# Performance work log

Hardware: AMD Instinct MI355X
Metric: run time of the kernel (lower is better)

Reference implementation:

```python
import jax, jax.numpy as jnp
import numpy as np

E = 8            # moe_num_experts
FFN = 8192       # ffn_hidden_size
D = 2048         # d_model
B, T = 1, 4096


def setup_inputs() -> dict:
    key = jax.random.key(0)
    k1, k2, k3, k4 = jax.random.split(key, 4)
    x = jax.random.normal(k1, (B, T, D), dtype=jnp.float32)
    # params stored flat as (E*FFN, D), as in the flax module
    w1 = jax.random.normal(k2, (E * FFN, D), dtype=jnp.float32) * 0.02
    v1 = jax.random.normal(k3, (E * FFN, D), dtype=jnp.float32) * 0.02
    w2 = jax.random.normal(k4, (E * FFN, D), dtype=jnp.float32) * 0.02
    return {"x": x, "w1": w1, "v1": v1, "w2": w2, "expert_idx": 3}


def reference(x, w1, v1, w2, expert_idx):
    # select this expert's weight slabs: (FFN, D) each
    expert_shape = (E, FFN, D)
    ew1 = w1.reshape(expert_shape)[expert_idx]
    ev1 = v1.reshape(expert_shape)[expert_idx]
    ew2 = w2.reshape(expert_shape)[expert_idx]
    # gate and up projections: [B,T,D] x [D,FFN] -> [B,T,FFN]
    x1 = jnp.einsum('btd,fd->btf', x, ew1)
    x2 = jnp.einsum('btd,fd->btf', x, ev1)
    h = jax.nn.silu(x1) * x2
    # down projection (note: matmul with ew2, i.e. contraction over FFN)
    out = jnp.einsum('btf,fd->btd', h, ew2)
    return out
```

## Files before the change

### kernel.cpp

```cpp
#include <hip/hip_runtime.h>

#define E_NUM 8
#define FFN_DIM 8192
#define D_DIM 2048
#define T_DIM 4096

using bf16x8 = __attribute__((ext_vector_type(8))) short;
using f32x4  = __attribute__((ext_vector_type(4))) float;
using u16x8  = __attribute__((ext_vector_type(8))) unsigned short;

__device__ __forceinline__ unsigned short f2bf(float f) {
  union { float f; unsigned int u; } v; v.f = f;
  unsigned int u = v.u;
  unsigned int r = (u + 0x7FFFu + ((u >> 16) & 1u)) >> 16;
  return (unsigned short)r;
}

__device__ __forceinline__ void gload16(const unsigned short* g, const unsigned short* l) {
  __builtin_amdgcn_global_load_lds(
      (const __attribute__((address_space(1))) void*)g,
      (__attribute__((address_space(3))) void*)l, 16, 0, 0);
}

__global__ void convert_kernel(const float* __restrict__ src_base,
                               const int* __restrict__ eidx, long slab,
                               unsigned short* __restrict__ dst, long n) {
  const float* src = src_base + (long)(*eidx) * slab;
  long stride = (long)gridDim.x * blockDim.x;
  for (long i = (long)blockIdx.x * blockDim.x + threadIdx.x; i * 8 < n; i += stride) {
    long e = i * 8;
    const float4* p = (const float4*)(src + e);
    float4 f0 = p[0], f1 = p[1];
    u16x8 o;
    o[0] = f2bf(f0.x); o[1] = f2bf(f0.y); o[2] = f2bf(f0.z); o[3] = f2bf(f0.w);
    o[4] = f2bf(f1.x); o[5] = f2bf(f1.y); o[6] = f2bf(f1.z); o[7] = f2bf(f1.w);
    *(u16x8*)(dst + e) = o;
  }
}

__global__ __launch_bounds__(512) void transpose_kernel(
    const float* __restrict__ w2, const int* __restrict__ eidx,
    unsigned short* __restrict__ dst) {
  __shared__ unsigned short tile[64][72];
  const float* src = w2 + (long)(*eidx) * (long)FFN_DIM * D_DIM;
  const int tid = threadIdx.x;
  int d0 = blockIdx.x << 6;
  int f0 = blockIdx.y << 6;
#pragma unroll
  for (int p = 0; p < 2; ++p) {
    int f = p * 32 + (tid >> 4);
    int dc = (tid & 15) * 4;
    float4 v = *(const float4*)(src + (long)(f0 + f) * D_DIM + d0 + dc);
    tile[f][dc + 0] = f2bf(v.x); tile[f][dc + 1] = f2bf(v.y);
    tile[f][dc + 2] = f2bf(v.z); tile[f][dc + 3] = f2bf(v.w);
  }
  __syncthreads();
  int d = tid >> 3;
  int fc = (tid & 7) * 8;
  u16x8 o;
#pragma unroll
  for (int j = 0; j < 8; ++j) o[j] = tile[fc + j][d];
  *(u16x8*)(dst + (long)(d0 + d) * FFN_DIM + f0 + fc) = o;
}

#define VMCNT8 asm volatile("s_waitcnt vmcnt(8)" ::: "memory")
#define VMCNT6 asm volatile("s_waitcnt vmcnt(6)" ::: "memory")
#define VMCNT5 asm volatile("s_waitcnt vmcnt(5)" ::: "memory")
#define VMCNT3 asm volatile("s_waitcnt vmcnt(3)" ::: "memory")
#define VMCNT0 asm volatile("s_waitcnt vmcnt(0)" ::: "memory")
#define BAR asm volatile("s_waitcnt lgkmcnt(0)\n\ts_barrier" ::: "memory")
#define PRIO1 __builtin_amdgcn_s_setprio(1)
#define PRIO0 __builtin_amdgcn_s_setprio(0)

__global__ __launch_bounds__(512, 2) void gemm1_silu(
    const unsigned short* __restrict__ Xb,
    const unsigned short* __restrict__ W1b,
    const unsigned short* __restrict__ V1b,
    unsigned short* __restrict__ Hb) {
  __shared__ __align__(16) unsigned short sA[2 * 16384];
  __shared__ __align__(16) unsigned short sB1[2 * 8192];
  __shared__ __align__(16) unsigned short sB2[2 * 8192];

  const int tid = threadIdx.x;
  const int wv = tid >> 6, l = tid & 63;
  const int wm = wv >> 2, wn = wv & 3;
  const int kq = l >> 4, lr = l & 15;
  const int bsw = (blockIdx.x & 7) * 128 + (blockIdx.x >> 3);
  const int m0 = (bsw >> 6) << 8;
  const int n0 = (bsw & 63) << 7;

  const int rsub = tid >> 3;
  const int sslot8 = ((tid & 7) ^ ((tid >> 3) & 7)) << 3;
  const unsigned short* gA  = Xb  + (long)(m0 + rsub) * D_DIM + sslot8;
  const unsigned short* gB1 = W1b + (long)(n0 + rsub) * D_DIM + sslot8;
  const unsigned short* gB2 = V1b + (long)(n0 + rsub) * D_DIM + sslot8;

#define STG1(gbase, r_, tc_, lbase) \
  gload16((gbase) + (long)((r_) * 64) * D_DIM + (tc_), (lbase) + (r_) * 4096 + wv * 512)

  int aoffA[4], aoffB[4], boff[2];
#pragma unroll
  for (int j = 0; j < 4; ++j) {
    int rowA = wm * 64 + j * 16 + lr;
    aoffA[j] = rowA * 64 + ((kq ^ (rowA & 7)) << 3);
    int rowB = 128 + wm * 64 + j * 16 + lr;
    aoffB[j] = rowB * 64 + ((kq ^ (rowB & 7)) << 3);
  }
#pragma unroll
  for (int g = 0; g < 2; ++g) {
    int row = wn * 32 + g * 16 + lr;
    boff[g] = row * 64 + ((kq ^ (row & 7)) << 3);
  }

  f32x4 acc1[8][2], acc2[8][2];
  f32x4 z = {0.f, 0.f, 0.f, 0.f};
#pragma unroll
  for (int f = 0; f < 8; ++f)
#pragma unroll
    for (int g = 0; g < 2; ++g) { acc1[f][g] = z; acc2[f][g] = z; }

  bf16x8 aA[4][2], aB[4][2], b1[2][2], b2[2][2];

  STG1(gB1, 0, 0, sB1); STG1(gB1, 1, 0, sB1);
  STG1(gA, 0, 0, sA); STG1(gA, 1, 0, sA); STG1(gA, 2, 0, sA); STG1(gA, 3, 0, sA);
  STG1(gB2, 0, 0, sB2); STG1(gB2, 1, 0, sB2);
  STG1(gB1, 0, 64, sB1 + 8192); STG1(gB1, 1, 64, sB1 + 8192);
  STG1(gA, 0, 64, sA + 16384); STG1(gA, 1, 64, sA + 16384);
  STG1(gA, 2, 64, sA + 16384); STG1(gA, 3, 64, sA + 16384);
  STG1(gB2, 0, 64, sB2 + 8192); STG1(gB2, 1, 64, sB2 + 8192);
  VMCNT8;
  BAR;
#pragma unroll
  for (int j = 0; j < 4; ++j) {
    aA[j][0] = *(const bf16x8*)(sA + aoffA[j]);
    aA[j][1] = *(const bf16x8*)(sA + (aoffA[j] ^ 32));
  }
#pragma unroll
  for (int g = 0; g < 2; ++g) {
    b1[g][0] = *(const bf16x8*)(sB1 + boff[g]);
    b1[g][1] = *(const bf16x8*)(sB1 + (boff[g] ^ 32));
  }
  BAR;

  const int NT = D_DIM / 64;
  for (int t = 0; t < NT; ++t) {
    const int db = t & 1, nx = db ^ 1;
    const unsigned short* Acur  = sA  + db * 16384;
    const unsigned short* Anxt  = sA  + nx * 16384;
    const unsigned short* B1nxt = sB1 + nx * 8192;
    const unsigned short* B2cur = sB2 + db * 8192;
    unsigned short* AcurW  = (unsigned short*)sA  + db * 16384;
    unsigned short* B1curW = (unsigned short*)sB1 + db * 8192;
    unsigned short* B2curW = (unsigned short*)sB2 + db * 8192;
    const int p1ok = (t + 1 < NT), p2ok = (t + 2 < NT);
    const int tc2 = (t + 2) << 6;

#pragma unroll
    for (int j = 0; j < 4; ++j) {
      aB[j][0] = *(const bf16x8*)(Acur + aoffB[j]);
      aB[j][1] = *(const bf16x8*)(Acur + (aoffB[j] ^ 32));
    }
    if (p2ok) { STG1(gB1, 0, tc2, B1curW); STG1(gB1, 1, tc2, B1curW); }
    PRIO1;
#pragma unroll
    for (int j = 0; j < 4; ++j)
#pragma unroll
      for (int g = 0; g < 2; ++g) {
        acc1[j][g] = __builtin_amdgcn_mfma_f32_16x16x32_bf16(aA[j][0], b1[g][0], acc1[j][g], 0, 0, 0);
        acc1[j][g] = __builtin_amdgcn_mfma_f32_16x16x32_bf16(aA[j][1], b1[g][1], acc1[j][g], 0, 0, 0);
      }
    PRIO0;
    BAR;

#pragma unroll
    for (int g = 0; g < 2; ++g) {
      b2[g][0] = *(const bf16x8*)(B2cur + boff[g]);
      b2[g][1] = *(const bf16x8*)(B2cur + (boff[g] ^ 32));
    }
    if (p2ok) { STG1(gA, 0, tc2, AcurW); STG1(gA, 1, tc2, AcurW); STG1(gA, 2, tc2, AcurW); }
    PRIO1;
#pragma unroll
    for (int j = 0; j < 4; ++j)
#pragma unroll
      for (int g = 0; g < 2; ++g) {
        acc1[4 + j][g] = __builtin_amdgcn_mfma_f32_16x16x32_bf16(aB[j][0], b1[g][0], acc1[4 + j][g], 0, 0, 0);
        acc1[4 + j][g] = __builtin_amdgcn_mfma_f32_16x16x32_bf16(aB[j][1], b1[g][1], acc1[4 + j][g], 0, 0, 0);
      }
    PRIO0;
    if (p2ok) { VMCNT5; } else if (p1ok) { VMCNT0; }
    BAR;

    if (p2ok) { STG1(gA, 3, tc2, AcurW); STG1(gB2, 0, tc2, B2curW); STG1(gB2, 1, tc2, B2curW); }
    PRIO1;
#pragma unroll
    for (int j = 0; j < 4; ++j)
#pragma unroll
      for (int g = 0; g < 2; ++g) {
        acc2[j][g] = __builtin_amdgcn_mfma_f32_16x16x32_bf16(aA[j][0], b2[g][0], acc2[j][g], 0, 0, 0);
        acc2[j][g] = __builtin_amdgcn_mfma_f32_16x16x32_bf16(aA[j][1], b2[g][1], acc2[j][g], 0, 0, 0);
      }
    PRIO0;
    if (p1ok) {
#pragma unroll
      for (int j = 0; j < 4; ++j) {
        aA[j][0] = *(const bf16x8*)(Anxt + aoffA[j]);
        aA[j][1] = *(const bf16x8*)(Anxt + (aoffA[j] ^ 32));
      }
    }
    BAR;

    PRIO1;
#pragma unroll
    for (int j = 0; j < 4; ++j)
#pragma unroll
      for (int g = 0; g < 2; ++g) {
        acc2[4 + j][g] = __builtin_amdgcn_mfma_f32_16x16x32_bf16(aB[j][0], b2[g][0], acc2[4 + j][g], 0, 0, 0);
        acc2[4 + j][g] = __builtin_amdgcn_mfma_f32_16x16x32_bf16(aB[j][1], b2[g][1], acc2[4 + j][g], 0, 0, 0);
      }
    PRIO0;
    if (p1ok) {
#pragma unroll
      for (int g = 0; g < 2; ++g) {
        b1[g][0] = *(const bf16x8*)(B1nxt + boff[g]);
        b1[g][1] = *(const bf16x8*)(B1nxt + (boff[g] ^ 32));
      }
    }
    BAR;
  }

#pragma unroll
  for (int f = 0; f < 8; ++f)
#pragma unroll
    for (int g = 0; g < 2; ++g)
#pragma unroll
      for (int r = 0; r < 4; ++r) {
        int row = m0 + (f >> 2) * 128 + wm * 64 + (f & 3) * 16 + kq * 4 + r;
        int col = n0 + wn * 32 + g * 16 + lr;
        float x1 = acc1[f][g][r], x2 = acc2[f][g][r];
        float hv = x1 / (1.f + __expf(-x1)) * x2;
        Hb[(long)row * FFN_DIM + col] = f2bf(hv);
      }
#undef STG1
}

__global__ __launch_bounds__(512, 2) void gemm2(
    const unsigned short* __restrict__ Hb,
    const unsigned short* __restrict__ W2T,
    float* __restrict__ out) {
  __shared__ __align__(16) unsigned short sA[2 * 16384];
  __shared__ __align__(16) unsigned short sB[2 * 8192];

  const int tid = threadIdx.x;
  const int wv = tid >> 6, l = tid & 63;
  const int wm = wv >> 1, wn = wv & 1;
  const int kq = l >> 4, lr = l & 15;
  const int bsw = (blockIdx.x & 7) * 32 + (blockIdx.x >> 3);
  const int m0 = (bsw >> 4) << 8;
  const int n0 = (bsw & 15) << 7;

  const int rsub = tid >> 3;
  const int sslot8 = ((tid & 7) ^ ((tid >> 3) & 7)) << 3;
  const unsigned short* gA = Hb  + (long)(m0 + rsub) * FFN_DIM + sslot8;
  const unsigned short* gB = W2T + (long)(n0 + rsub) * FFN_DIM + sslot8;

#define STG1(gbase, r_, tc_, lbase) \
  gload16((gbase) + (long)((r_) * 64) * FFN_DIM + (tc_), (lbase) + (r_) * 4096 + wv * 512)

  int aoff[4], boff[4];
#pragma unroll
  for (int f = 0; f < 4; ++f) {
    int row = wm * 64 + f * 16 + lr;
    aoff[f] = row * 64 + ((kq ^ (row & 7)) << 3);
  }
#pragma unroll
  for (int g = 0; g < 4; ++g) {
    int row = wn * 64 + g * 16 + lr;
    boff[g] = row * 64 + ((kq ^ (row & 7)) << 3);
  }

  f32x4 acc[4][4];
  f32x4 z = {0.f, 0.f, 0.f, 0.f};
#pragma unroll
  for (int f = 0; f < 4; ++f)
#pragma unroll
    for (int g = 0; g < 4; ++g) acc[f][g] = z;

  bf16x8 aA[2][2], aB[2][2], bA[2][2], bB[2][2];

  STG1(gB, 0, 0, sB); STG1(gB, 1, 0, sB);
  STG1(gA, 0, 0, sA); STG1(gA, 1, 0, sA); STG1(gA, 2, 0, sA); STG1(gA, 3, 0, sA);
  STG1(gB, 0, 64, sB + 8192); STG1(gB, 1, 64, sB + 8192);
  STG1(gA, 0, 64, sA + 16384); STG1(gA, 1, 64, sA + 16384);
  STG1(gA, 2, 64, sA + 16384); STG1(gA, 3, 64, sA + 16384);
  VMCNT6;
  BAR;
#pragma unroll
  for (int f = 0; f < 2; ++f) {
    aA[f][0] = *(const bf16x8*)(sA + aoff[f]);
    aA[f][1] = *(const bf16x8*)(sA + (aoff[f] ^ 32));
  }
#pragma unroll
  for (int g = 0; g < 2; ++g) {
    bA[g][0] = *(const bf16x8*)(sB + boff[g]);
    bA[g][1] = *(const bf16x8*)(sB + (boff[g] ^ 32));
  }
  BAR;

  const int NT = FFN_DIM / 64;
  for (int t = 0; t < NT; ++t) {
    const int db = t & 1, nx = db ^ 1;
    const unsigned short* Acur = sA + db * 16384;
    const unsigned short* Anxt = sA + nx * 16384;
    const unsigned short* Bcur = sB + db * 8192;
    const unsigned short* Bnxt = sB + nx * 8192;
    unsigned short* AcurW = (unsigned short*)sA + db * 16384;
    unsigned short* BcurW = (unsigned short*)sB + db * 8192;
    const int p1ok = (t + 1 < NT), p2ok = (t + 2 < NT);
    const int tc2 = (t + 2) << 6;

#pragma unroll
    for (int f = 0; f < 2; ++f) {
      aB[f][0] = *(const bf16x8*)(Acur + aoff[2 + f]);
      aB[f][1] = *(const bf16x8*)(Acur + (aoff[2 + f] ^ 32));
    }
#pragma unroll
    for (int g = 0; g < 2; ++g) {
      bB[g][0] = *(const bf16x8*)(Bcur + boff[2 + g]);
      bB[g][1] = *(const bf16x8*)(Bcur + (boff[2 + g] ^ 32));
    }
    PRIO1;
#pragma unroll
    for (int f = 0; f < 2; ++f)
#pragma unroll
      for (int g = 0; g < 2; ++g) {
        acc[f][g] = __builtin_amdgcn_mfma_f32_16x16x32_bf16(aA[f][0], bA[g][0], acc[f][g], 0, 0, 0);
        acc[f][g] = __builtin_amdgcn_mfma_f32_16x16x32_bf16(aA[f][1], bA[g][1], acc[f][g], 0, 0, 0);
      }
    PRIO0;
    BAR;

    if (p2ok) { STG1(gB, 0, tc2, BcurW); STG1(gB, 1, tc2, BcurW); STG1(gA, 0, tc2, AcurW); }
    PRIO1;
#pragma unroll
    for (int f = 0; f < 2; ++f)
#pragma unroll
      for (int g = 0; g < 2; ++g) {
        acc[2 + f][g] = __builtin_amdgcn_mfma_f32_16x16x32_bf16(aB[f][0], bA[g][0], acc[2 + f][g], 0, 0, 0);
        acc[2 + f][g] = __builtin_amdgcn_mfma_f32_16x16x32_bf16(aB[f][1], bA[g][1], acc[2 + f][g], 0, 0, 0);
      }
    PRIO0;
    if (p2ok) { VMCNT3; } else if (p1ok) { VMCNT0; }
    BAR;

    if (p2ok) { STG1(gA, 1, tc2, AcurW); STG1(gA, 2, tc2, AcurW); STG1(gA, 3, tc2, AcurW); }
    PRIO1;
#pragma unroll
    for (int f = 0; f < 2; ++f)
#pragma unroll
      for (int g = 0; g < 2; ++g) {
        acc[f][2 + g] = __builtin_amdgcn_mfma_f32_16x16x32_bf16(aA[f][0], bB[g][0], acc[f][2 + g], 0, 0, 0);
        acc[f][2 + g] = __builtin_amdgcn_mfma_f32_16x16x32_bf16(aA[f][1], bB[g][1], acc[f][2 + g], 0, 0, 0);
      }
    PRIO0;
    if (p1ok) {
#pragma unroll
      for (int f = 0; f < 2; ++f) {
        aA[f][0] = *(const bf16x8*)(Anxt + aoff[f]);
        aA[f][1] = *(const bf16x8*)(Anxt + (aoff[f] ^ 32));
      }
    }
    BAR;

    PRIO1;
#pragma unroll
    for (int f = 0; f < 2; ++f)
#pragma unroll
      for (int g = 0; g < 2; ++g) {
        acc[2 + f][2 + g] = __builtin_amdgcn_mfma_f32_16x16x32_bf16(aB[f][0], bB[g][0], acc[2 + f][2 + g], 0, 0, 0);
        acc[2 + f][2 + g] = __builtin_amdgcn_mfma_f32_16x16x32_bf16(aB[f][1], bB[g][1], acc[2 + f][2 + g], 0, 0, 0);
      }
    PRIO0;
    if (p1ok) {
#pragma unroll
      for (int g = 0; g < 2; ++g) {
        bA[g][0] = *(const bf16x8*)(Bnxt + boff[g]);
        bA[g][1] = *(const bf16x8*)(Bnxt + (boff[g] ^ 32));
      }
    }
    BAR;
  }

#pragma unroll
  for (int f = 0; f < 4; ++f)
#pragma unroll
    for (int g = 0; g < 4; ++g)
#pragma unroll
      for (int r = 0; r < 4; ++r) {
        int row = m0 + wm * 64 + f * 16 + kq * 4 + r;
        int col = n0 + wn * 64 + g * 16 + lr;
        out[(long)row * D_DIM + col] = acc[f][g][r];
      }
#undef STG1
}

extern "C" void kernel_launch(void* const* d_in, const int* in_sizes, int n_in,
                              void* d_out, int out_size, void* d_ws, size_t ws_size,
                              hipStream_t stream) {
  const float* x  = (const float*)d_in[0];
  const float* w1 = (const float*)d_in[1];
  const float* v1 = (const float*)d_in[2];
  const float* w2 = (const float*)d_in[3];
  const int* eidx = (const int*)d_in[4];

  char* ws = (char*)d_ws;
  unsigned short* Xb  = (unsigned short*)(ws);
  unsigned short* W1b = (unsigned short*)(ws + (16l << 20));
  unsigned short* V1b = (unsigned short*)(ws + (48l << 20));
  unsigned short* W2T = (unsigned short*)(ws + (80l << 20));
  unsigned short* Hb  = (unsigned short*)(ws + (112l << 20));
  float* out = (float*)d_out;

  long slab = (long)FFN_DIM * D_DIM;
  transpose_kernel<<<dim3(D_DIM / 64, FFN_DIM / 64), 512, 0, stream>>>(w2, eidx, W2T);
  convert_kernel<<<2048, 256, 0, stream>>>(w1, eidx, slab, W1b, slab);
  convert_kernel<<<2048, 256, 0, stream>>>(v1, eidx, slab, V1b, slab);
  convert_kernel<<<2048, 256, 0, stream>>>(x,  eidx, 0,    Xb,  (long)T_DIM * D_DIM);
  gemm1_silu<<<1024, 512, 0, stream>>>(Xb, W1b, V1b, Hb);
  gemm2<<<256, 512, 0, stream>>>(Hb, W2T, out);
}
```

Measured before the change: 486.5 us.

## Restructure GEMM main loops to load current-tile fragments and reorder async stages

Result: slower. 507.5 us (+4.3%).

```diff
diff --git a/kernel.cpp b/kernel.cpp
--- a/kernel.cpp
+++ b/kernel.cpp
@@ -63,12 +63,12 @@
   *(u16x8*)(dst + (long)(d0 + d) * FFN_DIM + f0 + fc) = o;
 }
 
-#define VMCNT8 asm volatile("s_waitcnt vmcnt(8)" ::: "memory")
 #define VMCNT6 asm volatile("s_waitcnt vmcnt(6)" ::: "memory")
 #define VMCNT5 asm volatile("s_waitcnt vmcnt(5)" ::: "memory")
-#define VMCNT3 asm volatile("s_waitcnt vmcnt(3)" ::: "memory")
 #define VMCNT0 asm volatile("s_waitcnt vmcnt(0)" ::: "memory")
-#define BAR asm volatile("s_waitcnt lgkmcnt(0)\n\ts_barrier" ::: "memory")
+#define BAR1  asm volatile("s_barrier" ::: "memory")
+#define LGKM0 asm volatile("s_waitcnt lgkmcnt(0)" ::: "memory")
+#define LGKM8 asm volatile("s_waitcnt lgkmcnt(8)" ::: "memory")
 #define PRIO1 __builtin_amdgcn_s_setprio(1)
 #define PRIO0 __builtin_amdgcn_s_setprio(0)
 
@@ -121,76 +121,80 @@
 
   bf16x8 aA[4][2], aB[4][2], b1[2][2], b2[2][2];
 
+  STG1(gA, 0, 0, sA); STG1(gA, 1, 0, sA);
   STG1(gB1, 0, 0, sB1); STG1(gB1, 1, 0, sB1);
-  STG1(gA, 0, 0, sA); STG1(gA, 1, 0, sA); STG1(gA, 2, 0, sA); STG1(gA, 3, 0, sA);
+  STG1(gA, 2, 0, sA); STG1(gA, 3, 0, sA);
   STG1(gB2, 0, 0, sB2); STG1(gB2, 1, 0, sB2);
+  STG1(gA, 0, 64, sA + 16384); STG1(gA, 1, 64, sA + 16384);
   STG1(gB1, 0, 64, sB1 + 8192); STG1(gB1, 1, 64, sB1 + 8192);
-  STG1(gA, 0, 64, sA + 16384); STG1(gA, 1, 64, sA + 16384);
   STG1(gA, 2, 64, sA + 16384); STG1(gA, 3, 64, sA + 16384);
-  STG1(gB2, 0, 64, sB2 + 8192); STG1(gB2, 1, 64, sB2 + 8192);
-  VMCNT8;
-  BAR;
-#pragma unroll
-  for (int j = 0; j < 4; ++j) {
-    aA[j][0] = *(const bf16x8*)(sA + aoffA[j]);
-    aA[j][1] = *(const bf16x8*)(sA + (aoffA[j] ^ 32));
-  }
-#pragma unroll
-  for (int g = 0; g < 2; ++g) {
-    b1[g][0] = *(const bf16x8*)(sB1 + boff[g]);
-    b1[g][1] = *(const bf16x8*)(sB1 + (boff[g] ^ 32));
-  }
-  BAR;
+  VMCNT6;
+  BAR1;
 
   const int NT = D_DIM / 64;
   for (int t = 0; t < NT; ++t) {
     const int db = t & 1, nx = db ^ 1;
     const unsigned short* Acur  = sA  + db * 16384;
-    const unsigned short* Anxt  = sA  + nx * 16384;
-    const unsigned short* B1nxt = sB1 + nx * 8192;
+    const unsigned short* B1cur = sB1 + db * 8192;
     const unsigned short* B2cur = sB2 + db * 8192;
-    unsigned short* AcurW  = (unsigned short*)sA  + db * 16384;
-    unsigned short* B1curW = (unsigned short*)sB1 + db * 8192;
-    unsigned short* B2curW = (unsigned short*)sB2 + db * 8192;
+    unsigned short* AdbW  = (unsigned short*)sA  + db * 16384;
+    unsigned short* B1dbW = (unsigned short*)sB1 + db * 8192;
+    unsigned short* B2nxW = (unsigned short*)sB2 + nx * 8192;
     const int p1ok = (t + 1 < NT), p2ok = (t + 2 < NT);
-    const int tc2 = (t + 2) << 6;
+    const int tc1 = (t + 1) << 6, tc2 = (t + 2) << 6;
+
+#pragma unroll
+    for (int j = 0; j < 4; ++j) {
+      aA[j][0] = *(const bf16x8*)(Acur + aoffA[j]);
+      aA[j][1] = *(const bf16x8*)(Acur + (aoffA[j] ^ 32));
+    }
+#pragma unroll
+    for (int g = 0; g < 2; ++g) {
+      b1[g][0] = *(const bf16x8*)(B1cur + boff[g]);
+      b1[g][1] = *(const bf16x8*)(B1cur + (boff[g] ^ 32));
+    }
+    if (p1ok) { STG1(gB2, 0, tc1, B2nxW); STG1(gB2, 1, tc1, B2nxW); }
+    LGKM8;
+    BAR1;
+    LGKM0;
+    PRIO1;
+#pragma unroll
+    for (int j = 0; j < 4; ++j)
+#pragma unroll
+      for (int g = 0; g < 2; ++g) {
+        acc1[j][g] = __builtin_amdgcn_mfma_f32_16x16x32_bf16(aA[j][0], b1[g][0], acc1[j][g], 0, 0, 0);
+        acc1[j][g] = __builtin_amdgcn_mfma_f32_16x16x32_bf16(aA[j][1], b1[g][1], acc1[j][g], 0, 0, 0);
+      }
+    PRIO0;
+    BAR1;
 
 #pragma unroll
     for (int j = 0; j < 4; ++j) {
       aB[j][0] = *(const bf16x8*)(Acur + aoffB[j]);
       aB[j][1] = *(const bf16x8*)(Acur + (aoffB[j] ^ 32));
     }
-    if (p2ok) { STG1(gB1, 0, tc2, B1curW); STG1(gB1, 1, tc2, B1curW); }
+    if (p2ok) { STG1(gA, 0, tc2, AdbW); STG1(gA, 1, tc2, AdbW); }
+    BAR1;
+    LGKM0;
     PRIO1;
 #pragma unroll
     for (int j = 0; j < 4; ++j)
 #pragma unroll
       for (int g = 0; g < 2; ++g) {
-        acc1[j][g] = __builtin_amdgcn_mfma_f32_16x16x32_bf16(aA[j][0], b1[g][0], acc1[j][g], 0, 0, 0);
-        acc1[j][g] = __builtin_amdgcn_mfma_f32_16x16x32_bf16(aA[j][1], b1[g][1], acc1[j][g], 0, 0, 0);
-      }
-    PRIO0;
-    BAR;
+        acc1[4 + j][g] = __builtin_amdgcn_mfma_f32_16x16x32_bf16(aB[j][0], b1[g][0], acc1[4 + j][g], 0, 0, 0);
+        acc1[4 + j][g] = __builtin_amdgcn_mfma_f32_16x16x32_bf16(aB[j][1], b1[g][1], acc1[4 + j][g], 0, 0, 0);
+      }
+    PRIO0;
+    BAR1;
 
 #pragma unroll
     for (int g = 0; g < 2; ++g) {
       b2[g][0] = *(const bf16x8*)(B2cur + boff[g]);
       b2[g][1] = *(const bf16x8*)(B2cur + (boff[g] ^ 32));
     }
-    if (p2ok) { STG1(gA, 0, tc2, AcurW); STG1(gA, 1, tc2, AcurW); STG1(gA, 2, tc2, AcurW); }
-    PRIO1;
-#pragma unroll
-    for (int j = 0; j < 4; ++j)
-#pragma unroll
-      for (int g = 0; g < 2; ++g) {
-        acc1[4 + j][g] = __builtin_amdgcn_mfma_f32_16x16x32_bf16(aB[j][0], b1[g][0], acc1[4 + j][g], 0, 0, 0);
-        acc1[4 + j][g] = __builtin_amdgcn_mfma_f32_16x16x32_bf16(aB[j][1], b1[g][1], acc1[4 + j][g], 0, 0, 0);
-      }
-    PRIO0;
-    if (p2ok) { VMCNT5; } else if (p1ok) { VMCNT0; }
-    BAR;
-
-    if (p2ok) { STG1(gA, 3, tc2, AcurW); STG1(gB2, 0, tc2, B2curW); STG1(gB2, 1, tc2, B2curW); }
+    if (p2ok) { STG1(gB1, 0, tc2, B1dbW); STG1(gB1, 1, tc2, B1dbW); }
+    BAR1;
+    LGKM0;
     PRIO1;
 #pragma unroll
     for (int j = 0; j < 4; ++j)
@@ -200,15 +204,10 @@
         acc2[j][g] = __builtin_amdgcn_mfma_f32_16x16x32_bf16(aA[j][1], b2[g][1], acc2[j][g], 0, 0, 0);
       }
     PRIO0;
-    if (p1ok) {
-#pragma unroll
-      for (int j = 0; j < 4; ++j) {
-        aA[j][0] = *(const bf16x8*)(Anxt + aoffA[j]);
-        aA[j][1] = *(const bf16x8*)(Anxt + (aoffA[j] ^ 32));
-      }
-    }
-    BAR;
-
+    BAR1;
+
+    if (p2ok) { STG1(gA, 2, tc2, AdbW); STG1(gA, 3, tc2, AdbW); }
+    BAR1;
     PRIO1;
 #pragma unroll
     for (int j = 0; j < 4; ++j)
@@ -218,14 +217,8 @@
         acc2[4 + j][g] = __builtin_amdgcn_mfma_f32_16x16x32_bf16(aB[j][1], b2[g][1], acc2[4 + j][g], 0, 0, 0);
       }
     PRIO0;
-    if (p1ok) {
-#pragma unroll
-      for (int g = 0; g < 2; ++g) {
-        b1[g][0] = *(const bf16x8*)(B1nxt + boff[g]);
-        b1[g][1] = *(const bf16x8*)(B1nxt + (boff[g] ^ 32));
-      }
-    }
-    BAR;
+    if (p2ok) { VMCNT6; } else if (p1ok) { VMCNT0; }
+    BAR1;
   }
 
 #pragma unroll
@@ -287,72 +280,76 @@
 
   bf16x8 aA[2][2], aB[2][2], bA[2][2], bB[2][2];
 
+  STG1(gA, 0, 0, sA); STG1(gA, 1, 0, sA);
+  STG1(gA, 2, 0, sA); STG1(gA, 3, 0, sA);
   STG1(gB, 0, 0, sB); STG1(gB, 1, 0, sB);
-  STG1(gA, 0, 0, sA); STG1(gA, 1, 0, sA); STG1(gA, 2, 0, sA); STG1(gA, 3, 0, sA);
-  STG1(gB, 0, 64, sB + 8192); STG1(gB, 1, 64, sB + 8192);
   STG1(gA, 0, 64, sA + 16384); STG1(gA, 1, 64, sA + 16384);
   STG1(gA, 2, 64, sA + 16384); STG1(gA, 3, 64, sA + 16384);
-  VMCNT6;
-  BAR;
-#pragma unroll
-  for (int f = 0; f < 2; ++f) {
-    aA[f][0] = *(const bf16x8*)(sA + aoff[f]);
-    aA[f][1] = *(const bf16x8*)(sA + (aoff[f] ^ 32));
-  }
-#pragma unroll
-  for (int g = 0; g < 2; ++g) {
-    bA[g][0] = *(const bf16x8*)(sB + boff[g]);
-    bA[g][1] = *(const bf16x8*)(sB + (boff[g] ^ 32));
-  }
-  BAR;
+  STG1(gB, 0, 64, sB + 8192);
+  VMCNT5;
+  BAR1;
 
   const int NT = FFN_DIM / 64;
   for (int t = 0; t < NT; ++t) {
     const int db = t & 1, nx = db ^ 1;
     const unsigned short* Acur = sA + db * 16384;
-    const unsigned short* Anxt = sA + nx * 16384;
     const unsigned short* Bcur = sB + db * 8192;
-    const unsigned short* Bnxt = sB + nx * 8192;
-    unsigned short* AcurW = (unsigned short*)sA + db * 16384;
-    unsigned short* BcurW = (unsigned short*)sB + db * 8192;
+    unsigned short* AdbW = (unsigned short*)sA + db * 16384;
+    unsigned short* BdbW = (unsigned short*)sB + db * 8192;
+    unsigned short* BnxW = (unsigned short*)sB + nx * 8192;
     const int p1ok = (t + 1 < NT), p2ok = (t + 2 < NT);
-    const int tc2 = (t + 2) << 6;
+    const int tc1 = (t + 1) << 6, tc2 = (t + 2) << 6;
+
+#pragma unroll
+    for (int f = 0; f < 2; ++f) {
+      aA[f][0] = *(const bf16x8*)(Acur + aoff[f]);
+      aA[f][1] = *(const bf16x8*)(Acur + (aoff[f] ^ 32));
+    }
+#pragma unroll
+    for (int g = 0; g < 2; ++g) {
+      bA[g][0] = *(const bf16x8*)(Bcur + boff[g]);
+      bA[g][1] = *(const bf16x8*)(Bcur + (boff[g] ^ 32));
+    }
+    if (p1ok) { STG1(gB, 1, tc1, BnxW); }
+    BAR1;
+    LGKM0;
+    PRIO1;
+#pragma unroll
+    for (int f = 0; f < 2; ++f)
+#pragma unroll
+      for (int g = 0; g < 2; ++g) {
+        acc[f][g] = __builtin_amdgcn_mfma_f32_16x16x32_bf16(aA[f][0], bA[g][0], acc[f][g], 0, 0, 0);
+        acc[f][g] = __builtin_amdgcn_mfma_f32_16x16x32_bf16(aA[f][1], bA[g][1], acc[f][g], 0, 0, 0);
+      }
+    PRIO0;
+    BAR1;
 
 #pragma unroll
     for (int f = 0; f < 2; ++f) {
       aB[f][0] = *(const bf16x8*)(Acur + aoff[2 + f]);
       aB[f][1] = *(const bf16x8*)(Acur + (aoff[2 + f] ^ 32));
     }
+    BAR1;
+    LGKM0;
+    PRIO1;
+#pragma unroll
+    for (int f = 0; f < 2; ++f)
+#pragma unroll
+      for (int g = 0; g < 2; ++g) {
+        acc[2 + f][g] = __builtin_amdgcn_mfma_f32_16x16x32_bf16(aB[f][0], bA[g][0], acc[2 + f][g], 0, 0, 0);
+        acc[2 + f][g] = __builtin_amdgcn_mfma_f32_16x16x32_bf16(aB[f][1], bA[g][1], acc[2 + f][g], 0, 0, 0);
+      }
+    PRIO0;
+    BAR1;
+
 #pragma unroll
     for (int g = 0; g < 2; ++g) {
       bB[g][0] = *(const bf16x8*)(Bcur + boff[2 + g]);
       bB[g][1] = *(const bf16x8*)(Bcur + (boff[2 + g] ^ 32));
     }
-    PRIO1;
-#pragma unroll
-    for (int f = 0; f < 2; ++f)
-#pragma unroll
-      for (int g = 0; g < 2; ++g) {
-        acc[f][g] = __builtin_amdgcn_mfma_f32_16x16x32_bf16(aA[f][0], bA[g][0], acc[f][g], 0, 0, 0);
-        acc[f][g] = __builtin_amdgcn_mfma_f32_16x16x32_bf16(aA[f][1], bA[g][1], acc[f][g], 0, 0, 0);
-      }
-    PRIO0;
-    BAR;
-
-    if (p2ok) { STG1(gB, 0, tc2, BcurW); STG1(gB, 1, tc2, BcurW); STG1(gA, 0, tc2, AcurW); }
-    PRIO1;
-#pragma unroll
-    for (int f = 0; f < 2; ++f)
-#pragma unroll
-      for (int g = 0; g < 2; ++g) {
-        acc[2 + f][g] = __builtin_amdgcn_mfma_f32_16x16x32_bf16(aB[f][0], bA[g][0], acc[2 + f][g], 0, 0, 0);
-        acc[2 + f][g] = __builtin_amdgcn_mfma_f32_16x16x32_bf16(aB[f][1], bA[g][1], acc[2 + f][g], 0, 0, 0);
-      }
-    PRIO0;
-    if (p2ok) { VMCNT3; } else if (p1ok) { VMCNT0; }
-    BAR;
-
-    if (p2ok) { STG1(gA, 1, tc2, AcurW); STG1(gA, 2, tc2, AcurW); STG1(gA, 3, tc2, AcurW); }
+    if (p2ok) { STG1(gA, 0, tc2, AdbW); STG1(gA, 1, tc2, AdbW); }
+    BAR1;
+    LGKM0;
     PRIO1;
 #pragma unroll
     for (int f = 0; f < 2; ++f)
@@ -362,15 +359,10 @@
         acc[f][2 + g] = __builtin_amdgcn_mfma_f32_16x16x32_bf16(aA[f][1], bB[g][1], acc[f][2 + g], 0, 0, 0);
       }
     PRIO0;
-    if (p1ok) {
-#pragma unroll
-      for (int f = 0; f < 2; ++f) {
-        aA[f][0] = *(const bf16x8*)(Anxt + aoff[f]);
-        aA[f][1] = *(const bf16x8*)(Anxt + (aoff[f] ^ 32));
-      }
-    }
-    BAR;
-
+    BAR1;
+
+    if (p2ok) { STG1(gA, 2, tc2, AdbW); STG1(gA, 3, tc2, AdbW); STG1(gB, 0, tc2, BdbW); }
+    BAR1;
     PRIO1;
 #pragma unroll
     for (int f = 0; f < 2; ++f)
@@ -380,14 +372,8 @@
         acc[2 + f][2 + g] = __builtin_amdgcn_mfma_f32_16x16x32_bf16(aB[f][1], bB[g][1], acc[2 + f][2 + g], 0, 0, 0);
       }
     PRIO0;
-    if (p1ok) {
-#pragma unroll
-      for (int g = 0; g < 2; ++g) {
-        bA[g][0] = *(const bf16x8*)(Bnxt + boff[g]);
-        bA[g][1] = *(const bf16x8*)(Bnxt + (boff[g] ^ 32));
-      }
-    }
-    BAR;
+    if (p2ok) { VMCNT5; } else if (p1ok) { VMCNT0; }
+    BAR1;
   }
 
 #pragma unroll
```

## Restructure gate/up GEMM as fused wide-N tile with LDS SiLU epilogue

Applied to the files above, without the earlier changes.

New measurement: 494.5 us. About the same (+1.6%).

```diff
diff --git a/kernel.cpp b/kernel.cpp
--- a/kernel.cpp
+++ b/kernel.cpp
@@ -63,12 +63,12 @@
   *(u16x8*)(dst + (long)(d0 + d) * FFN_DIM + f0 + fc) = o;
 }
 
-#define VMCNT8 asm volatile("s_waitcnt vmcnt(8)" ::: "memory")
 #define VMCNT6 asm volatile("s_waitcnt vmcnt(6)" ::: "memory")
-#define VMCNT5 asm volatile("s_waitcnt vmcnt(5)" ::: "memory")
 #define VMCNT3 asm volatile("s_waitcnt vmcnt(3)" ::: "memory")
 #define VMCNT0 asm volatile("s_waitcnt vmcnt(0)" ::: "memory")
-#define BAR asm volatile("s_waitcnt lgkmcnt(0)\n\ts_barrier" ::: "memory")
+#define BARX  asm volatile("s_barrier" ::: "memory")
+#define LGKM0 asm volatile("s_waitcnt lgkmcnt(0)" ::: "memory")
+#define BARD asm volatile("s_waitcnt lgkmcnt(0)\n\ts_barrier" ::: "memory")
 #define PRIO1 __builtin_amdgcn_s_setprio(1)
 #define PRIO0 __builtin_amdgcn_s_setprio(0)
 
@@ -77,9 +77,9 @@
     const unsigned short* __restrict__ W1b,
     const unsigned short* __restrict__ V1b,
     unsigned short* __restrict__ Hb) {
-  __shared__ __align__(16) unsigned short sA[2 * 16384];
-  __shared__ __align__(16) unsigned short sB1[2 * 8192];
-  __shared__ __align__(16) unsigned short sB2[2 * 8192];
+  __shared__ __align__(16) unsigned short lds[65536];
+  unsigned short* sA = lds;
+  unsigned short* sB = lds + 32768;
 
   const int tid = threadIdx.x;
   const int wv = tid >> 6, l = tid & 63;
@@ -87,160 +87,163 @@
   const int kq = l >> 4, lr = l & 15;
   const int bsw = (blockIdx.x & 7) * 128 + (blockIdx.x >> 3);
   const int m0 = (bsw >> 6) << 8;
-  const int n0 = (bsw & 63) << 7;
+  const int ffn0 = (bsw & 63) << 7;
 
   const int rsub = tid >> 3;
-  const int sslot8 = ((tid & 7) ^ ((tid >> 3) & 7)) << 3;
-  const unsigned short* gA  = Xb  + (long)(m0 + rsub) * D_DIM + sslot8;
-  const unsigned short* gB1 = W1b + (long)(n0 + rsub) * D_DIM + sslot8;
-  const unsigned short* gB2 = V1b + (long)(n0 + rsub) * D_DIM + sslot8;
-
-#define STG1(gbase, r_, tc_, lbase) \
-  gload16((gbase) + (long)((r_) * 64) * D_DIM + (tc_), (lbase) + (r_) * 4096 + wv * 512)
-
-  int aoffA[4], aoffB[4], boff[2];
-#pragma unroll
-  for (int j = 0; j < 4; ++j) {
-    int rowA = wm * 64 + j * 16 + lr;
-    aoffA[j] = rowA * 64 + ((kq ^ (rowA & 7)) << 3);
-    int rowB = 128 + wm * 64 + j * 16 + lr;
-    aoffB[j] = rowB * 64 + ((kq ^ (rowB & 7)) << 3);
-  }
-#pragma unroll
-  for (int g = 0; g < 2; ++g) {
-    int row = wn * 32 + g * 16 + lr;
-    boff[g] = row * 64 + ((kq ^ (row & 7)) << 3);
-  }
-
-  f32x4 acc1[8][2], acc2[8][2];
+  const int slotg = ((tid & 7) ^ (rsub & 7)) << 3;
+  const unsigned short* gA  = Xb  + (long)(m0 + rsub) * D_DIM + slotg;
+  const unsigned short* gB1 = W1b + (long)(ffn0 + rsub) * D_DIM + slotg;
+  const unsigned short* gB2 = V1b + (long)(ffn0 + rsub) * D_DIM + slotg;
+
+#define SGA(db, h, r_, tc_) \
+  gload16(gA + (long)((h) * 128 + (r_) * 64) * D_DIM + (tc_), \
+          sA + (db) * 16384 + (h) * 8192 + (r_) * 4096 + wv * 512)
+#define SGB1(db, r_, tc_) \
+  gload16(gB1 + (long)((r_) * 64) * D_DIM + (tc_), \
+          sB + (db) * 16384 + (r_) * 4096 + wv * 512)
+#define SGB2(db, r_, tc_) \
+  gload16(gB2 + (long)((r_) * 64) * D_DIM + (tc_), \
+          sB + (db) * 16384 + 8192 + (r_) * 4096 + wv * 512)
+
+  int aoff[8], boff[4];
+#pragma unroll
+  for (int j = 0; j < 8; ++j) {
+    int row = wm * 128 + j * 16 + lr;
+    aoff[j] = row * 64 + ((kq ^ (row & 7)) << 3);
+  }
+#pragma unroll
+  for (int n = 0; n < 4; ++n) {
+    int row = wn * 64 + n * 16 + lr;
+    boff[n] = row * 64 + ((kq ^ (row & 7)) << 3);
+  }
+
+  f32x4 acc[8][4];
   f32x4 z = {0.f, 0.f, 0.f, 0.f};
 #pragma unroll
-  for (int f = 0; f < 8; ++f)
-#pragma unroll
-    for (int g = 0; g < 2; ++g) { acc1[f][g] = z; acc2[f][g] = z; }
-
-  bf16x8 aA[4][2], aB[4][2], b1[2][2], b2[2][2];
-
-  STG1(gB1, 0, 0, sB1); STG1(gB1, 1, 0, sB1);
-  STG1(gA, 0, 0, sA); STG1(gA, 1, 0, sA); STG1(gA, 2, 0, sA); STG1(gA, 3, 0, sA);
-  STG1(gB2, 0, 0, sB2); STG1(gB2, 1, 0, sB2);
-  STG1(gB1, 0, 64, sB1 + 8192); STG1(gB1, 1, 64, sB1 + 8192);
-  STG1(gA, 0, 64, sA + 16384); STG1(gA, 1, 64, sA + 16384);
-  STG1(gA, 2, 64, sA + 16384); STG1(gA, 3, 64, sA + 16384);
-  STG1(gB2, 0, 64, sB2 + 8192); STG1(gB2, 1, 64, sB2 + 8192);
-  VMCNT8;
-  BAR;
-#pragma unroll
-  for (int j = 0; j < 4; ++j) {
-    aA[j][0] = *(const bf16x8*)(sA + aoffA[j]);
-    aA[j][1] = *(const bf16x8*)(sA + (aoffA[j] ^ 32));
-  }
-#pragma unroll
-  for (int g = 0; g < 2; ++g) {
-    b1[g][0] = *(const bf16x8*)(sB1 + boff[g]);
-    b1[g][1] = *(const bf16x8*)(sB1 + (boff[g] ^ 32));
-  }
-  BAR;
-
-  const int NT = D_DIM / 64;
-  for (int t = 0; t < NT; ++t) {
-    const int db = t & 1, nx = db ^ 1;
-    const unsigned short* Acur  = sA  + db * 16384;
-    const unsigned short* Anxt  = sA  + nx * 16384;
-    const unsigned short* B1nxt = sB1 + nx * 8192;
-    const unsigned short* B2cur = sB2 + db * 8192;
-    unsigned short* AcurW  = (unsigned short*)sA  + db * 16384;
-    unsigned short* B1curW = (unsigned short*)sB1 + db * 8192;
-    unsigned short* B2curW = (unsigned short*)sB2 + db * 8192;
-    const int p1ok = (t + 1 < NT), p2ok = (t + 2 < NT);
-    const int tc2 = (t + 2) << 6;
-
-#pragma unroll
-    for (int j = 0; j < 4; ++j) {
-      aB[j][0] = *(const bf16x8*)(Acur + aoffB[j]);
-      aB[j][1] = *(const bf16x8*)(Acur + (aoffB[j] ^ 32));
-    }
-    if (p2ok) { STG1(gB1, 0, tc2, B1curW); STG1(gB1, 1, tc2, B1curW); }
-    PRIO1;
-#pragma unroll
-    for (int j = 0; j < 4; ++j)
-#pragma unroll
-      for (int g = 0; g < 2; ++g) {
-        acc1[j][g] = __builtin_amdgcn_mfma_f32_16x16x32_bf16(aA[j][0], b1[g][0], acc1[j][g], 0, 0, 0);
-        acc1[j][g] = __builtin_amdgcn_mfma_f32_16x16x32_bf16(aA[j][1], b1[g][1], acc1[j][g], 0, 0, 0);
-      }
-    PRIO0;
-    BAR;
-
-#pragma unroll
-    for (int g = 0; g < 2; ++g) {
-      b2[g][0] = *(const bf16x8*)(B2cur + boff[g]);
-      b2[g][1] = *(const bf16x8*)(B2cur + (boff[g] ^ 32));
-    }
-    if (p2ok) { STG1(gA, 0, tc2, AcurW); STG1(gA, 1, tc2, AcurW); STG1(gA, 2, tc2, AcurW); }
-    PRIO1;
-#pragma unroll
-    for (int j = 0; j < 4; ++j)
-#pragma unroll
-      for (int g = 0; g < 2; ++g) {
-        acc1[4 + j][g] = __builtin_amdgcn_mfma_f32_16x16x32_bf16(aB[j][0], b1[g][0], acc1[4 + j][g], 0, 0, 0);
-        acc1[4 + j][g] = __builtin_amdgcn_mfma_f32_16x16x32_bf16(aB[j][1], b1[g][1], acc1[4 + j][g], 0, 0, 0);
-      }
-    PRIO0;
-    if (p2ok) { VMCNT5; } else if (p1ok) { VMCNT0; }
-    BAR;
-
-    if (p2ok) { STG1(gA, 3, tc2, AcurW); STG1(gB2, 0, tc2, B2curW); STG1(gB2, 1, tc2, B2curW); }
-    PRIO1;
-#pragma unroll
-    for (int j = 0; j < 4; ++j)
-#pragma unroll
-      for (int g = 0; g < 2; ++g) {
-        acc2[j][g] = __builtin_amdgcn_mfma_f32_16x16x32_bf16(aA[j][0], b2[g][0], acc2[j][g], 0, 0, 0);
-        acc2[j][g] = __builtin_amdgcn_mfma_f32_16x16x32_bf16(aA[j][1], b2[g][1], acc2[j][g], 0, 0, 0);
-      }
-    PRIO0;
-    if (p1ok) {
-#pragma unroll
-      for (int j = 0; j < 4; ++j) {
-        aA[j][0] = *(const bf16x8*)(Anxt + aoffA[j]);
-        aA[j][1] = *(const bf16x8*)(Anxt + (aoffA[j] ^ 32));
-      }
-    }
-    BAR;
-
-    PRIO1;
-#pragma unroll
-    for (int j = 0; j < 4; ++j)
-#pragma unroll
-      for (int g = 0; g < 2; ++g) {
-        acc2[4 + j][g] = __builtin_amdgcn_mfma_f32_16x16x32_bf16(aB[j][0], b2[g][0], acc2[4 + j][g], 0, 0, 0);
-        acc2[4 + j][g] = __builtin_amdgcn_mfma_f32_16x16x32_bf16(aB[j][1], b2[g][1], acc2[4 + j][g], 0, 0, 0);
-      }
-    PRIO0;
-    if (p1ok) {
-#pragma unroll
-      for (int g = 0; g < 2; ++g) {
-        b1[g][0] = *(const bf16x8*)(B1nxt + boff[g]);
-        b1[g][1] = *(const bf16x8*)(B1nxt + (boff[g] ^ 32));
-      }
-    }
-    BAR;
-  }
-
-#pragma unroll
-  for (int f = 0; f < 8; ++f)
-#pragma unroll
-    for (int g = 0; g < 2; ++g)
-#pragma unroll
-      for (int r = 0; r < 4; ++r) {
-        int row = m0 + (f >> 2) * 128 + wm * 64 + (f & 3) * 16 + kq * 4 + r;
-        int col = n0 + wn * 32 + g * 16 + lr;
-        float x1 = acc1[f][g][r], x2 = acc2[f][g][r];
-        float hv = x1 / (1.f + __expf(-x1)) * x2;
-        Hb[(long)row * FFN_DIM + col] = f2bf(hv);
-      }
-#undef STG1
+  for (int j = 0; j < 8; ++j)
+#pragma unroll
+    for (int n = 0; n < 4; ++n) acc[j][n] = z;
+
+  bf16x8 aX[4][2], bLo[2][2], bHi[2][2];
+
+  SGB1(0, 0, 0); SGB1(0, 1, 0);
+  SGB2(0, 0, 0); SGB2(0, 1, 0);
+  SGA(0, 0, 0, 0); SGA(0, 0, 1, 0);
+  SGA(0, 1, 0, 0); SGA(0, 1, 1, 0);
+  SGB1(1, 0, 64); SGB1(1, 1, 64);
+  SGB2(1, 0, 64); SGB2(1, 1, 64);
+  SGA(1, 0, 0, 64); SGA(1, 0, 1, 64);
+  VMCNT6;
+  BARX;
+
+#define RD_A(J0, base) \
+  _Pragma("unroll") for (int j = 0; j < 4; ++j) { \
+    aX[j][0] = *(const bf16x8*)((base) + aoff[(J0) + j]); \
+    aX[j][1] = *(const bf16x8*)((base) + (aoff[(J0) + j] ^ 32)); }
+#define RD_B(dst, N0, base) \
+  _Pragma("unroll") for (int n = 0; n < 2; ++n) { \
+    dst[n][0] = *(const bf16x8*)((base) + boff[(N0) + n]); \
+    dst[n][1] = *(const bf16x8*)((base) + (boff[(N0) + n] ^ 32)); }
+#define MFMA_Q(J0, N0, br) \
+  PRIO1; \
+  _Pragma("unroll") for (int j = 0; j < 4; ++j) \
+  _Pragma("unroll") for (int n = 0; n < 2; ++n) { \
+    acc[(J0)+j][(N0)+n] = __builtin_amdgcn_mfma_f32_16x16x32_bf16(aX[j][0], br[n][0], acc[(J0)+j][(N0)+n], 0, 0, 0); \
+    acc[(J0)+j][(N0)+n] = __builtin_amdgcn_mfma_f32_16x16x32_bf16(aX[j][1], br[n][1], acc[(J0)+j][(N0)+n], 0, 0, 0); } \
+  PRIO0;
+
+  const int NITER = D_DIM / 128;
+  for (int i = 0; i < NITER; ++i) {
+    const unsigned short* cA = sA;
+    const unsigned short* cB = sB;
+    const unsigned short* nA = sA + 16384;
+    const unsigned short* nB = sB + 16384;
+    const int tcn = (2 * i + 1) << 6;
+    const int tc2 = (2 * i + 2) << 6;
+    const int tc3 = (2 * i + 3) << 6;
+    const int st2 = (2 * i + 2 < 32), st3 = (2 * i + 3 < 32);
+
+    RD_A(0, cA); RD_B(bLo, 0, cB);
+    SGA(1, 1, 0, tcn); SGA(1, 1, 1, tcn);
+    BARX; LGKM0;
+    MFMA_Q(0, 0, bLo);
+    BARX;
+
+    RD_B(bHi, 2, cB);
+    BARX; LGKM0;
+    MFMA_Q(0, 2, bHi);
+    BARX;
+
+    RD_A(4, cA);
+    if (st2) { SGB1(0, 0, tc2); SGB1(0, 1, tc2); }
+    BARX; LGKM0;
+    MFMA_Q(4, 2, bHi);
+    BARX;
+
+    if (st2) { SGB2(0, 0, tc2); SGB2(0, 1, tc2); SGA(0, 0, 0, tc2); SGA(0, 0, 1, tc2); }
+    BARX;
+    MFMA_Q(4, 0, bLo);
+    if (st2) { VMCNT6; } else { VMCNT0; }
+    BARX;
+
+    RD_A(0, nA); RD_B(bLo, 0, nB);
+    if (st2) { SGA(0, 1, 0, tc2); SGA(0, 1, 1, tc2); }
+    BARX; LGKM0;
+    MFMA_Q(0, 0, bLo);
+    BARX;
+
+    RD_B(bHi, 2, nB);
+    BARX; LGKM0;
+    MFMA_Q(0, 2, bHi);
+    BARX;
+
+    RD_A(4, nA);
+    if (st3) { SGB1(1, 0, tc3); SGB1(1, 1, tc3); }
+    BARX; LGKM0;
+    MFMA_Q(4, 2, bHi);
+    BARX;
+
+    if (st3) { SGB2(1, 0, tc3); SGB2(1, 1, tc3); SGA(1, 0, 0, tc3); SGA(1, 0, 1, tc3); }
+    BARX;
+    MFMA_Q(4, 0, bLo);
+    if (st3) { VMCNT6; } else { VMCNT0; }
+    BARX;
+  }
+
+  float* xls = (float*)lds;
+  if (wn >= 2) {
+    const int base = (wm * 2 + (wn - 2)) * 8192;
+#pragma unroll
+    for (int j = 0; j < 8; ++j)
+#pragma unroll
+      for (int n = 0; n < 4; ++n)
+#pragma unroll
+        for (int r = 0; r < 4; ++r)
+          xls[base + (j * 16 + kq * 4 + r) * 64 + n * 16 + lr] = acc[j][n][r];
+  }
+  BARD;
+  if (wn < 2) {
+    const int base = (wm * 2 + wn) * 8192;
+#pragma unroll
+    for (int j = 0; j < 8; ++j)
+#pragma unroll
+      for (int n = 0; n < 4; ++n)
+#pragma unroll
+        for (int r = 0; r < 4; ++r) {
+          float x1 = acc[j][n][r];
+          float x2 = xls[base + (j * 16 + kq * 4 + r) * 64 + n * 16 + lr];
+          float hv = x1 / (1.f + __expf(-x1)) * x2;
+          int row = m0 + wm * 128 + j * 16 + kq * 4 + r;
+          int col = ffn0 + wn * 64 + n * 16 + lr;
+          Hb[(long)row * FFN_DIM + col] = f2bf(hv);
+        }
+  }
+#undef SGA
+#undef SGB1
+#undef SGB2
+#undef RD_A
+#undef RD_B
+#undef MFMA_Q
 }
 
 __global__ __launch_bounds__(512, 2) void gemm2(
@@ -293,7 +296,7 @@
   STG1(gA, 0, 64, sA + 16384); STG1(gA, 1, 64, sA + 16384);
   STG1(gA, 2, 64, sA + 16384); STG1(gA, 3, 64, sA + 16384);
   VMCNT6;
-  BAR;
+  BARD;
 #pragma unroll
   for (int f = 0; f < 2; ++f) {
     aA[f][0] = *(const bf16x8*)(sA + aoff[f]);
@@ -304,7 +307,7 @@
     bA[g][0] = *(const bf16x8*)(sB + boff[g]);
     bA[g][1] = *(const bf16x8*)(sB + (boff[g] ^ 32));
   }
-  BAR;
+  BARD;
 
   const int NT = FFN_DIM / 64;
   for (int t = 0; t < NT; ++t) {
@@ -337,7 +340,7 @@
         acc[f][g] = __builtin_amdgcn_mfma_f32_16x16x32_bf16(aA[f][1], bA[g][1], acc[f][g], 0, 0, 0);
       }
     PRIO0;
-    BAR;
+    BARD;
 
     if (p2ok) { STG1(gB, 0, tc2, BcurW); STG1(gB, 1, tc2, BcurW); STG1(gA, 0, tc2, AcurW); }
     PRIO1;
@@ -350,7 +353,7 @@
       }
     PRIO0;
     if (p2ok) { VMCNT3; } else if (p1ok) { VMCNT0; }
-    BAR;
+    BARD;
 
     if (p2ok) { STG1(gA, 1, tc2, AcurW); STG1(gA, 2, tc2, AcurW); STG1(gA, 3, tc2, AcurW); }
     PRIO1;
@@ -369,7 +372,7 @@
         aA[f][1] = *(const bf16x8*)(Anxt + (aoff[f] ^ 32));
       }
     }
-    BAR;
+    BARD;
 
     PRIO1;
 #pragma unroll
@@ -387,7 +390,7 @@
         bA[g][1] = *(const bf16x8*)(Bnxt + (boff[g] ^ 32));
       }
     }
-    BAR;
+    BARD;
   }
 
 #pragma unroll
```
